# Optimization experiments

Measured on AMD Instinct MI355X. Metric: run time of the kernel, lower is better.

## Reference

```python
import jax, jax.numpy as jnp
import numpy as np

B, S, D, H = 2, 2048, 768, 12
HD = D // H


def setup_inputs() -> dict:
    key = jax.random.key(0)
    ks = jax.random.split(key, 11)
    scale = 1.0 / np.sqrt(D)
    return {
        "query": jax.random.normal(ks[0], (B, S, D), jnp.float32),
        "key_": jax.random.normal(ks[1], (B, S, D), jnp.float32),
        "value": jax.random.normal(ks[2], (B, S, D), jnp.float32),
        "Wq": jax.random.normal(ks[3], (D, D), jnp.float32) * scale,
        "bq": jnp.zeros((D,), jnp.float32),
        "Wk": jax.random.normal(ks[4], (D, D), jnp.float32) * scale,
        "bk": jnp.zeros((D,), jnp.float32),
        "Wv": jax.random.normal(ks[5], (D, D), jnp.float32) * scale,
        "bv": jnp.zeros((D,), jnp.float32),
        "Wo": jax.random.normal(ks[6], (D, D), jnp.float32) * scale,
        "bo": jnp.zeros((D,), jnp.float32),
    }


def reference(query, key_, value, Wq, bq, Wk, bk, Wv, bv, Wo, bo):
    # Linear projections (W stored as [in, out]); dropout = identity (eval)
    def split_heads(x):
        # [B, S, D] -> [B, H, S, HD]
        return x.reshape(B, S, H, HD).transpose(0, 2, 1, 3)

    Q = split_heads(query @ Wq + bq)
    K = split_heads(key_ @ Wk + bk)
    V = split_heads(value @ Wv + bv)

    inv_sqrt_dk = 1.0 / jnp.sqrt(jnp.asarray(HD, Q.dtype))
    score = jnp.einsum("bhqd,bhkd->bhqk", Q, K) * inv_sqrt_dk  # [B,H,S,S]
    prob = jax.nn.softmax(score, axis=-1)  # source bug: mask is never applied
    out = jnp.einsum("bhqk,bhkd->bhqd", prob, V)  # [B,H,S,HD]
    out = out.transpose(0, 2, 1, 3).reshape(B, S, D)
    return out @ Wo + bo
```

## Files before the change

### kernel.cpp

```cpp
#include <hip/hip_runtime.h>
#include <hip/hip_bf16.h>

#define BB 2
#define SS 2048
#define DDIM 768
#define NH 12
#define HD 64
#define MTOT (BB*SS)

constexpr float QSCALE = 0.125f * 1.44269504088896340736f;

typedef __bf16 bf16_t;
typedef __bf16 bf16x8 __attribute__((ext_vector_type(8)));
typedef __bf16 bf16x4 __attribute__((ext_vector_type(4)));
typedef float  f32x4  __attribute__((ext_vector_type(4)));

static __device__ __forceinline__ f32x4 mfma16(bf16x8 a, bf16x8 b, f32x4 c) {
    return __builtin_amdgcn_mfma_f32_16x16x32_bf16(a, b, c, 0, 0, 0);
}

typedef __attribute__((address_space(3))) unsigned int lds_u32;
typedef __attribute__((address_space(1))) const unsigned int glob_u32;
static __device__ __forceinline__ void gload16(const bf16_t* g, bf16_t* l) {
    __builtin_amdgcn_global_load_lds((glob_u32*)g, (lds_u32*)l, 16, 0, 0);
}

__global__ __launch_bounds__(256) void prep_all(
    const float* __restrict__ Wq, const float* __restrict__ Wk,
    const float* __restrict__ Wv, const float* __restrict__ Wo,
    const float* __restrict__ q, const float* __restrict__ k_,
    bf16_t* __restrict__ Wt, bf16_t* __restrict__ Xb)
{
    const int z = blockIdx.z, tid = threadIdx.x;
    if (z < 4) {
        if (blockIdx.x >= 24 || blockIdx.y >= 24) return;
        __shared__ float tile[32][33];
        const float* W = (z == 0) ? Wq : (z == 1) ? Wk : (z == 2) ? Wv : Wo;
        int n0 = blockIdx.x * 32, k0 = blockIdx.y * 32;
        int tx = tid & 31, ty = tid >> 5;
#pragma unroll
        for (int i = 0; i < 4; i++) {
            int k = ty + i * 8;
            tile[k][tx] = W[(size_t)(k0 + k) * DDIM + n0 + tx];
        }
        __syncthreads();
        bf16_t* out = Wt + (size_t)z * DDIM * DDIM;
#pragma unroll
        for (int i = 0; i < 4; i++) {
            int n = ty + i * 8;
            out[(size_t)(n0 + n) * DDIM + k0 + tx] = (bf16_t)tile[tx][n];
        }
    } else {
        const float* src = (z == 4) ? q : k_;
        size_t base = ((size_t)(blockIdx.y * 48 + blockIdx.x)) * 2048 + (size_t)tid * 8;
        f32x4 v0 = *(const f32x4*)&src[base];
        f32x4 v1 = *(const f32x4*)&src[base + 4];
        bf16x8 o;
#pragma unroll
        for (int i = 0; i < 4; i++) { o[i] = (bf16_t)v0[i]; o[i + 4] = (bf16_t)v1[i]; }
        *(bf16x8*)&Xb[(size_t)(z - 4) * MTOT * DDIM + base] = o;
    }
}

__global__ __launch_bounds__(256) void gemm_qkv(
    const bf16_t* __restrict__ Xb, const float* __restrict__ vf,
    const float* __restrict__ bq, const float* __restrict__ bk, const float* __restrict__ bv,
    const bf16_t* __restrict__ Wt,
    bf16_t* __restrict__ Q, bf16_t* __restrict__ K, bf16_t* __restrict__ Vtg)
{
    __shared__ alignas(16) bf16_t As[128 * 32];
    __shared__ alignas(16) bf16_t Bs[128 * 32];
    const int z = blockIdx.z;
    const int m0 = blockIdx.y * 128, n0 = blockIdx.x * 128;
    const int tid = threadIdx.x, lane = tid & 63, w = tid >> 6;
    const int wm = (w >> 1) * 64, wn = (w & 1) * 64;
    const int quad = lane >> 4, l15 = lane & 15;

    const bf16_t* A  = Xb + (size_t)z * (MTOT * DDIM);
    const bf16_t* Bt = Wt + (size_t)z * (DDIM * DDIM);
    const int srow = w * 32 + (lane >> 2);
    const int sg   = ((lane & 3) ^ ((lane >> 3) & 3)) * 8;
    bf16_t* AsW = &As[w * 1024];
    bf16_t* BsW = &Bs[w * 1024];
    const int frow = tid >> 1, fhalf = tid & 1;

    f32x4 acc[4][4];
#pragma unroll
    for (int mt = 0; mt < 4; mt++)
#pragma unroll
        for (int nt = 0; nt < 4; nt++) { f32x4 zz = {0.f,0.f,0.f,0.f}; acc[mt][nt] = zz; }

    const int aslot = (quad ^ ((l15 >> 1) & 3)) * 8;

    for (int k0 = 0; k0 < DDIM; k0 += 32) {
        __syncthreads();
        if (z < 2) {
            const bf16_t* Ag = A + (size_t)(m0 + srow) * DDIM + k0 + sg;
            gload16(Ag, AsW);
            gload16(Ag + (size_t)16 * DDIM, AsW + 512);
        } else {
            const float* src = vf + (size_t)(m0 + frow) * DDIM + k0 + fhalf * 16;
            f32x4 v0 = *(const f32x4*)(src);
            f32x4 v1 = *(const f32x4*)(src + 4);
            f32x4 v2 = *(const f32x4*)(src + 8);
            f32x4 v3 = *(const f32x4*)(src + 12);
            bf16x8 o0, o1;
#pragma unroll
            for (int i = 0; i < 4; i++) {
                o0[i] = (bf16_t)v0[i]; o0[i + 4] = (bf16_t)v1[i];
                o1[i] = (bf16_t)v2[i]; o1[i + 4] = (bf16_t)v3[i];
            }
            int sw = (frow >> 1) & 3;
            *(bf16x8*)&As[frow * 32 + ((2 * fhalf)     ^ sw) * 8] = o0;
            *(bf16x8*)&As[frow * 32 + ((2 * fhalf + 1) ^ sw) * 8] = o1;
        }
        {
            const bf16_t* Bg = Bt + (size_t)(n0 + srow) * DDIM + k0 + sg;
            gload16(Bg, BsW);
            gload16(Bg + (size_t)16 * DDIM, BsW + 512);
        }
        __syncthreads();

        bf16x8 a[4], b[4];
#pragma unroll
        for (int mt = 0; mt < 4; mt++)
            a[mt] = *(const bf16x8*)&As[(wm + mt * 16 + l15) * 32 + aslot];
#pragma unroll
        for (int nt = 0; nt < 4; nt++)
            b[nt] = *(const bf16x8*)&Bs[(wn + nt * 16 + l15) * 32 + aslot];
#pragma unroll
        for (int mt = 0; mt < 4; mt++)
#pragma unroll
            for (int nt = 0; nt < 4; nt++)
                acc[mt][nt] = mfma16(a[mt], b[nt], acc[mt][nt]);
    }

    const float* bias = (z == 0) ? bq : (z == 1) ? bk : bv;
    float bvals[4];
#pragma unroll
    for (int nt = 0; nt < 4; nt++)
        bvals[nt] = bias[n0 + wn + nt * 16 + l15];

    if (z == 2) {
#pragma unroll
        for (int mt = 0; mt < 4; mt++) {
            int row0 = m0 + wm + mt * 16 + quad * 4;
#pragma unroll
            for (int nt = 0; nt < 4; nt++) {
                int col = n0 + wn + nt * 16 + l15;
                bf16x4 pk;
#pragma unroll
                for (int r = 0; r < 4; r++) pk[r] = (bf16_t)(acc[mt][nt][r] + bvals[nt]);
                *(bf16x4*)&Vtg[(size_t)col * MTOT + row0] = pk;
            }
        }
    } else {
        bf16_t* C = (z == 0) ? Q : K;
        float scale = (z == 0) ? QSCALE : 1.0f;
#pragma unroll
        for (int mt = 0; mt < 4; mt++) {
            int row0 = m0 + wm + mt * 16 + quad * 4;
#pragma unroll
            for (int nt = 0; nt < 4; nt++) {
                int col = n0 + wn + nt * 16 + l15;
#pragma unroll
                for (int r = 0; r < 4; r++)
                    C[(size_t)(row0 + r) * DDIM + col] = (bf16_t)((acc[mt][nt][r] + bvals[nt]) * scale);
            }
        }
    }
}

__global__ __launch_bounds__(256) void gemm_out(
    const bf16_t* __restrict__ Ab, const bf16_t* __restrict__ Bt,
    const float* __restrict__ bo, float* __restrict__ out)
{
    __shared__ alignas(16) bf16_t As[128 * 32];
    __shared__ alignas(16) bf16_t Bs[128 * 32];
    const int m0 = blockIdx.y * 128, n0 = blockIdx.x * 128;
    const int tid = threadIdx.x, lane = tid & 63, w = tid >> 6;
    const int wm = (w >> 1) * 64, wn = (w & 1) * 64;
    const int quad = lane >> 4, l15 = lane & 15;
    const int srow = w * 32 + (lane >> 2);
    const int sg   = ((lane & 3) ^ ((lane >> 3) & 3)) * 8;
    bf16_t* AsW = &As[w * 1024];
    bf16_t* BsW = &Bs[w * 1024];

    f32x4 acc[4][4];
#pragma unroll
    for (int mt = 0; mt < 4; mt++)
#pragma unroll
        for (int nt = 0; nt < 4; nt++) { f32x4 zz = {0.f,0.f,0.f,0.f}; acc[mt][nt] = zz; }

    const int aslot = (quad ^ ((l15 >> 1) & 3)) * 8;

    for (int k0 = 0; k0 < DDIM; k0 += 32) {
        __syncthreads();
        const bf16_t* Ag = Ab + (size_t)(m0 + srow) * DDIM + k0 + sg;
        gload16(Ag, AsW);
        gload16(Ag + (size_t)16 * DDIM, AsW + 512);
        const bf16_t* Bg = Bt + (size_t)(n0 + srow) * DDIM + k0 + sg;
        gload16(Bg, BsW);
        gload16(Bg + (size_t)16 * DDIM, BsW + 512);
        __syncthreads();

        bf16x8 a[4], b[4];
#pragma unroll
        for (int mt = 0; mt < 4; mt++)
            a[mt] = *(const bf16x8*)&As[(wm + mt * 16 + l15) * 32 + aslot];
#pragma unroll
        for (int nt = 0; nt < 4; nt++)
            b[nt] = *(const bf16x8*)&Bs[(wn + nt * 16 + l15) * 32 + aslot];
#pragma unroll
        for (int mt = 0; mt < 4; mt++)
#pragma unroll
            for (int nt = 0; nt < 4; nt++)
                acc[mt][nt] = mfma16(a[mt], b[nt], acc[mt][nt]);
    }

    float bvals[4];
#pragma unroll
    for (int nt = 0; nt < 4; nt++)
        bvals[nt] = bo[n0 + wn + nt * 16 + l15];
#pragma unroll
    for (int mt = 0; mt < 4; mt++) {
        int row0 = m0 + wm + mt * 16 + quad * 4;
#pragma unroll
        for (int nt = 0; nt < 4; nt++) {
            int col = n0 + wn + nt * 16 + l15;
#pragma unroll
            for (int r = 0; r < 4; r++)
                out[(size_t)(row0 + r) * DDIM + col] = acc[mt][nt][r] + bvals[nt];
        }
    }
}

__global__ __launch_bounds__(256) void attn_kernel(
    const bf16_t* __restrict__ Qb, const bf16_t* __restrict__ Kb,
    const bf16_t* __restrict__ Vtg, bf16_t* __restrict__ Ab)
{
    const int id = blockIdx.x;
    const int hb = id % 24, qi = id / 24;
    const int h = hb % NH, b = hb / NH;
    const int q0 = qi * 64;
    const int tid = threadIdx.x, lane = tid & 63, w = tid >> 6;
    const int quad = lane >> 4, l15 = lane & 15;

    __shared__ union {
        struct {
            alignas(16) bf16_t Ps[64][144];
        } a;
        struct {
            alignas(16) float Obuf[2][64][68];
            float Lb[4][64];
        } m;
    } u;

    bf16x8 qf[4][2];
#pragma unroll
    for (int qt = 0; qt < 4; qt++) {
        const bf16_t* src = Qb + (size_t)(b * SS + q0 + qt * 16 + l15) * DDIM + h * HD;
#pragma unroll
        for (int kh = 0; kh < 2; kh++)
            qf[qt][kh] = *(const bf16x8*)(src + kh * 32 + quad * 8);
    }

    f32x4 o[4][4];
#pragma unroll
    for (int dt = 0; dt < 4; dt++)
#pragma unroll
        for (int qt = 0; qt < 4; qt++) { f32x4 z = {0.f,0.f,0.f,0.f}; o[dt][qt] = z; }
    float l_s[4];
#pragma unroll
    for (int qt = 0; qt < 4; qt++) l_s[qt] = 0.f;

    const bf16_t* kfrag = Kb + (size_t)(b * SS + w * 32 + l15) * DDIM + h * HD + quad * 8;
    const bf16_t* vfrag = Vtg + (size_t)(h * HD + l15) * MTOT + b * SS + w * 32 + quad * 8;

    for (int kt0 = 0; kt0 < SS; kt0 += 128) {
        f32x4 s_[2][4];
#pragma unroll
        for (int kt = 0; kt < 2; kt++) {
            const bf16_t* kr = kfrag + (size_t)(kt0 + kt * 16) * DDIM;
            bf16x8 ak0 = *(const bf16x8*)(kr);
            bf16x8 ak1 = *(const bf16x8*)(kr + 32);
#pragma unroll
            for (int qt = 0; qt < 4; qt++) {
                f32x4 z = {0.f,0.f,0.f,0.f};
                z = mfma16(ak0, qf[qt][0], z);
                z = mfma16(ak1, qf[qt][1], z);
                s_[kt][qt] = z;
            }
        }

#pragma unroll
        for (int qt = 0; qt < 4; qt++) {
            float rs = l_s[qt];
#pragma unroll
            for (int kt = 0; kt < 2; kt++) {
                bf16x4 pk;
#pragma unroll
                for (int r = 0; r < 4; r++) {
                    float p = __builtin_amdgcn_exp2f(s_[kt][qt][r]);
                    rs += p;
                    pk[r] = (bf16_t)p;
                }
                *(bf16x4*)&u.a.Ps[qt * 16 + l15][w * 32 + kt * 16 + quad * 4] = pk;
            }
            l_s[qt] = rs;
        }

        bf16x8 av8[4], bp[4];
#pragma unroll
        for (int dt = 0; dt < 4; dt++)
            av8[dt] = *(const bf16x8*)(vfrag + (size_t)(dt * 16) * MTOT + kt0);
#pragma unroll
        for (int qt = 0; qt < 4; qt++)
            bp[qt] = *(const bf16x8*)&u.a.Ps[qt * 16 + l15][w * 32 + quad * 8];
#pragma unroll
        for (int dt = 0; dt < 4; dt++)
#pragma unroll
            for (int qt = 0; qt < 4; qt++)
                o[dt][qt] = mfma16(av8[dt], bp[qt], o[dt][qt]);
    }

#pragma unroll
    for (int qt = 0; qt < 4; qt++) {
        float rs = l_s[qt];
        rs += __shfl_xor(rs, 16, 64);
        rs += __shfl_xor(rs, 32, 64);
        l_s[qt] = rs;
    }
    __syncthreads();
    if (quad == 0) {
#pragma unroll
        for (int qt = 0; qt < 4; qt++)
            u.m.Lb[w][qt * 16 + l15] = l_s[qt];
    }
    __syncthreads();
    float lstar[4];
#pragma unroll
    for (int qt = 0; qt < 4; qt++) {
        int q = qt * 16 + l15;
        lstar[qt] = u.m.Lb[0][q] + u.m.Lb[1][q] + u.m.Lb[2][q] + u.m.Lb[3][q];
    }
    if (w >= 2) {
        float* dst = &u.m.Obuf[w - 2][lane][0];
#pragma unroll
        for (int dt = 0; dt < 4; dt++)
#pragma unroll
            for (int qt = 0; qt < 4; qt++)
                *(f32x4*)(dst + (dt * 4 + qt) * 4) = o[dt][qt];
    }
    __syncthreads();
    if (w < 2) {
        const float* src = &u.m.Obuf[w][lane][0];
#pragma unroll
        for (int dt = 0; dt < 4; dt++)
#pragma unroll
            for (int qt = 0; qt < 4; qt++)
                o[dt][qt] += *(const f32x4*)(src + (dt * 4 + qt) * 4);
    }
    __syncthreads();
    if (w == 1) {
        float* dst = &u.m.Obuf[0][lane][0];
#pragma unroll
        for (int dt = 0; dt < 4; dt++)
#pragma unroll
            for (int qt = 0; qt < 4; qt++)
                *(f32x4*)(dst + (dt * 4 + qt) * 4) = o[dt][qt];
    }
    __syncthreads();
    if (w == 0) {
        const float* src = &u.m.Obuf[0][lane][0];
#pragma unroll
        for (int dt = 0; dt < 4; dt++)
#pragma unroll
            for (int qt = 0; qt < 4; qt++)
                o[dt][qt] += *(const f32x4*)(src + (dt * 4 + qt) * 4);
#pragma unroll
        for (int qt = 0; qt < 4; qt++) {
            float inv = 1.f / lstar[qt];
            size_t rbase = (size_t)(b * SS + q0 + qt * 16 + l15) * DDIM + h * HD;
#pragma unroll
            for (int dt = 0; dt < 4; dt++) {
                bf16x4 pk;
#pragma unroll
                for (int r = 0; r < 4; r++) pk[r] = (bf16_t)(o[dt][qt][r] * inv);
                *(bf16x4*)&Ab[rbase + dt * 16 + quad * 4] = pk;
            }
        }
    }
}

extern "C" void kernel_launch(void* const* d_in, const int* in_sizes, int n_in,
                              void* d_out, int out_size, void* d_ws, size_t ws_size,
                              hipStream_t stream)
{
    const float* q  = (const float*)d_in[0];
    const float* k  = (const float*)d_in[1];
    const float* v  = (const float*)d_in[2];
    const float* Wq = (const float*)d_in[3];
    const float* bq = (const float*)d_in[4];
    const float* Wk = (const float*)d_in[5];
    const float* bk = (const float*)d_in[6];
    const float* Wv = (const float*)d_in[7];
    const float* bv = (const float*)d_in[8];
    const float* Wo = (const float*)d_in[9];
    const float* bo = (const float*)d_in[10];
    float* out = (float*)d_out;

    bf16_t* Wt  = (bf16_t*)d_ws;
    bf16_t* Xb  = Wt + (size_t)4 * DDIM * DDIM;
    bf16_t* Qs  = Xb + (size_t)2 * MTOT * DDIM;
    bf16_t* Ks  = Qs + (size_t)MTOT * DDIM;
    bf16_t* Vtg = Ks + (size_t)MTOT * DDIM;
    bf16_t* Ab  = Xb;

    prep_all<<<dim3(48, 32, 6), 256, 0, stream>>>(Wq, Wk, Wv, Wo, q, k, Wt, Xb);
    gemm_qkv<<<dim3(6, 32, 3), 256, 0, stream>>>(Xb, v, bq, bk, bv, Wt, Qs, Ks, Vtg);
    attn_kernel<<<dim3((SS / 64) * NH * BB), 256, 0, stream>>>(Qs, Ks, Vtg, Ab);
    gemm_out<<<dim3(6, 32), 256, 0, stream>>>(Ab, Wt + (size_t)3 * DDIM * DDIM, bo, out);
}
```

Before: 213.6 us.

## Fuse fp32→bf16 input conversion into QKV GEMM and software-pipeline attention loop

The separate pass that converted query and key activations to bf16 is dropped. The QKV GEMM now reads fp32 for all three projections and converts them in registers, as it already did for value. The attention loop is also software-pipelined: the P·V product for the previous key tile is issued alongside the QK^T for the current tile, with V fragments prefetched one iteration ahead. The fused conversion removes a full write-then-read round trip of the activations but drops the async global_load_lds path for Q/K, and the pipelining raises register pressure.

```diff
diff --git a/kernel.cpp b/kernel.cpp
--- a/kernel.cpp
+++ b/kernel.cpp
@@ -25,45 +25,32 @@
     __builtin_amdgcn_global_load_lds((glob_u32*)g, (lds_u32*)l, 16, 0, 0);
 }
 
-__global__ __launch_bounds__(256) void prep_all(
+__global__ __launch_bounds__(256) void prep_w(
     const float* __restrict__ Wq, const float* __restrict__ Wk,
     const float* __restrict__ Wv, const float* __restrict__ Wo,
-    const float* __restrict__ q, const float* __restrict__ k_,
-    bf16_t* __restrict__ Wt, bf16_t* __restrict__ Xb)
+    bf16_t* __restrict__ Wt)
 {
     const int z = blockIdx.z, tid = threadIdx.x;
-    if (z < 4) {
-        if (blockIdx.x >= 24 || blockIdx.y >= 24) return;
-        __shared__ float tile[32][33];
-        const float* W = (z == 0) ? Wq : (z == 1) ? Wk : (z == 2) ? Wv : Wo;
-        int n0 = blockIdx.x * 32, k0 = blockIdx.y * 32;
-        int tx = tid & 31, ty = tid >> 5;
-#pragma unroll
-        for (int i = 0; i < 4; i++) {
-            int k = ty + i * 8;
-            tile[k][tx] = W[(size_t)(k0 + k) * DDIM + n0 + tx];
-        }
-        __syncthreads();
-        bf16_t* out = Wt + (size_t)z * DDIM * DDIM;
-#pragma unroll
-        for (int i = 0; i < 4; i++) {
-            int n = ty + i * 8;
-            out[(size_t)(n0 + n) * DDIM + k0 + tx] = (bf16_t)tile[tx][n];
-        }
-    } else {
-        const float* src = (z == 4) ? q : k_;
-        size_t base = ((size_t)(blockIdx.y * 48 + blockIdx.x)) * 2048 + (size_t)tid * 8;
-        f32x4 v0 = *(const f32x4*)&src[base];
-        f32x4 v1 = *(const f32x4*)&src[base + 4];
-        bf16x8 o;
-#pragma unroll
-        for (int i = 0; i < 4; i++) { o[i] = (bf16_t)v0[i]; o[i + 4] = (bf16_t)v1[i]; }
-        *(bf16x8*)&Xb[(size_t)(z - 4) * MTOT * DDIM + base] = o;
+    __shared__ float tile[32][33];
+    const float* W = (z == 0) ? Wq : (z == 1) ? Wk : (z == 2) ? Wv : Wo;
+    int n0 = blockIdx.x * 32, k0 = blockIdx.y * 32;
+    int tx = tid & 31, ty = tid >> 5;
+#pragma unroll
+    for (int i = 0; i < 4; i++) {
+        int k = ty + i * 8;
+        tile[k][tx] = W[(size_t)(k0 + k) * DDIM + n0 + tx];
+    }
+    __syncthreads();
+    bf16_t* out = Wt + (size_t)z * DDIM * DDIM;
+#pragma unroll
+    for (int i = 0; i < 4; i++) {
+        int n = ty + i * 8;
+        out[(size_t)(n0 + n) * DDIM + k0 + tx] = (bf16_t)tile[tx][n];
     }
 }
 
 __global__ __launch_bounds__(256) void gemm_qkv(
-    const bf16_t* __restrict__ Xb, const float* __restrict__ vf,
+    const float* __restrict__ qf_, const float* __restrict__ kf_, const float* __restrict__ vf_,
     const float* __restrict__ bq, const float* __restrict__ bk, const float* __restrict__ bv,
     const bf16_t* __restrict__ Wt,
     bf16_t* __restrict__ Q, bf16_t* __restrict__ K, bf16_t* __restrict__ Vtg)
@@ -76,11 +63,10 @@
     const int wm = (w >> 1) * 64, wn = (w & 1) * 64;
     const int quad = lane >> 4, l15 = lane & 15;
 
-    const bf16_t* A  = Xb + (size_t)z * (MTOT * DDIM);
+    const float* A = (z == 0) ? qf_ : (z == 1) ? kf_ : vf_;
     const bf16_t* Bt = Wt + (size_t)z * (DDIM * DDIM);
     const int srow = w * 32 + (lane >> 2);
     const int sg   = ((lane & 3) ^ ((lane >> 3) & 3)) * 8;
-    bf16_t* AsW = &As[w * 1024];
     bf16_t* BsW = &Bs[w * 1024];
     const int frow = tid >> 1, fhalf = tid & 1;
 
@@ -94,12 +80,8 @@
 
     for (int k0 = 0; k0 < DDIM; k0 += 32) {
         __syncthreads();
-        if (z < 2) {
-            const bf16_t* Ag = A + (size_t)(m0 + srow) * DDIM + k0 + sg;
-            gload16(Ag, AsW);
-            gload16(Ag + (size_t)16 * DDIM, AsW + 512);
-        } else {
-            const float* src = vf + (size_t)(m0 + frow) * DDIM + k0 + fhalf * 16;
+        {
+            const float* src = A + (size_t)(m0 + frow) * DDIM + k0 + fhalf * 16;
             f32x4 v0 = *(const f32x4*)(src);
             f32x4 v1 = *(const f32x4*)(src + 4);
             f32x4 v2 = *(const f32x4*)(src + 8);
@@ -277,22 +259,25 @@
     const bf16_t* kfrag = Kb + (size_t)(b * SS + w * 32 + l15) * DDIM + h * HD + quad * 8;
     const bf16_t* vfrag = Vtg + (size_t)(h * HD + l15) * MTOT + b * SS + w * 32 + quad * 8;
 
-    for (int kt0 = 0; kt0 < SS; kt0 += 128) {
+    bf16x8 vp[4];
+#pragma unroll
+    for (int dt = 0; dt < 4; dt++)
+        vp[dt] = *(const bf16x8*)(vfrag + (size_t)(dt * 16) * MTOT);
+    {
         f32x4 s_[2][4];
 #pragma unroll
         for (int kt = 0; kt < 2; kt++) {
-            const bf16_t* kr = kfrag + (size_t)(kt0 + kt * 16) * DDIM;
+            const bf16_t* kr = kfrag + (size_t)(kt * 16) * DDIM;
             bf16x8 ak0 = *(const bf16x8*)(kr);
             bf16x8 ak1 = *(const bf16x8*)(kr + 32);
 #pragma unroll
             for (int qt = 0; qt < 4; qt++) {
-                f32x4 z = {0.f,0.f,0.f,0.f};
-                z = mfma16(ak0, qf[qt][0], z);
-                z = mfma16(ak1, qf[qt][1], z);
-                s_[kt][qt] = z;
-            }
-        }
-
+                f32x4 zz = {0.f,0.f,0.f,0.f};
+                zz = mfma16(ak0, qf[qt][0], zz);
+                zz = mfma16(ak1, qf[qt][1], zz);
+                s_[kt][qt] = zz;
+            }
+        }
 #pragma unroll
         for (int qt = 0; qt < 4; qt++) {
             float rs = l_s[qt];
@@ -309,19 +294,72 @@
             }
             l_s[qt] = rs;
         }
-
-        bf16x8 av8[4], bp[4];
-#pragma unroll
-        for (int dt = 0; dt < 4; dt++)
-            av8[dt] = *(const bf16x8*)(vfrag + (size_t)(dt * 16) * MTOT + kt0);
+    }
+
+    for (int kt0 = 128; kt0 < SS; kt0 += 128) {
+        bf16x8 ak[2][2];
+#pragma unroll
+        for (int kt = 0; kt < 2; kt++) {
+            const bf16_t* kr = kfrag + (size_t)(kt0 + kt * 16) * DDIM;
+            ak[kt][0] = *(const bf16x8*)(kr);
+            ak[kt][1] = *(const bf16x8*)(kr + 32);
+        }
+        bf16x8 bp[4];
 #pragma unroll
         for (int qt = 0; qt < 4; qt++)
             bp[qt] = *(const bf16x8*)&u.a.Ps[qt * 16 + l15][w * 32 + quad * 8];
-#pragma unroll
-        for (int dt = 0; dt < 4; dt++)
-#pragma unroll
-            for (int qt = 0; qt < 4; qt++)
-                o[dt][qt] = mfma16(av8[dt], bp[qt], o[dt][qt]);
+        bf16x8 vc[4];
+#pragma unroll
+        for (int dt = 0; dt < 4; dt++)
+            vc[dt] = *(const bf16x8*)(vfrag + (size_t)(dt * 16) * MTOT + kt0);
+
+#pragma unroll
+        for (int dt = 0; dt < 4; dt++)
+#pragma unroll
+            for (int qt = 0; qt < 4; qt++)
+                o[dt][qt] = mfma16(vp[dt], bp[qt], o[dt][qt]);
+
+        f32x4 s_[2][4];
+#pragma unroll
+        for (int kt = 0; kt < 2; kt++) {
+#pragma unroll
+            for (int qt = 0; qt < 4; qt++) {
+                f32x4 zz = {0.f,0.f,0.f,0.f};
+                zz = mfma16(ak[kt][0], qf[qt][0], zz);
+                zz = mfma16(ak[kt][1], qf[qt][1], zz);
+                s_[kt][qt] = zz;
+            }
+        }
+#pragma unroll
+        for (int qt = 0; qt < 4; qt++) {
+            float rs = l_s[qt];
+#pragma unroll
+            for (int kt = 0; kt < 2; kt++) {
+                bf16x4 pk;
+#pragma unroll
+                for (int r = 0; r < 4; r++) {
+                    float p = __builtin_amdgcn_exp2f(s_[kt][qt][r]);
+                    rs += p;
+                    pk[r] = (bf16_t)p;
+                }
+                *(bf16x4*)&u.a.Ps[qt * 16 + l15][w * 32 + kt * 16 + quad * 4] = pk;
+            }
+            l_s[qt] = rs;
+        }
+#pragma unroll
+        for (int dt = 0; dt < 4; dt++) vp[dt] = vc[dt];
+    }
+
+    {
+        bf16x8 bp[4];
+#pragma unroll
+        for (int qt = 0; qt < 4; qt++)
+            bp[qt] = *(const bf16x8*)&u.a.Ps[qt * 16 + l15][w * 32 + quad * 8];
+#pragma unroll
+        for (int dt = 0; dt < 4; dt++)
+#pragma unroll
+            for (int qt = 0; qt < 4; qt++)
+                o[dt][qt] = mfma16(vp[dt], bp[qt], o[dt][qt]);
     }
 
 #pragma unroll
@@ -411,14 +449,13 @@
     float* out = (float*)d_out;
 
     bf16_t* Wt  = (bf16_t*)d_ws;
-    bf16_t* Xb  = Wt + (size_t)4 * DDIM * DDIM;
-    bf16_t* Qs  = Xb + (size_t)2 * MTOT * DDIM;
+    bf16_t* Qs  = Wt + (size_t)4 * DDIM * DDIM;
     bf16_t* Ks  = Qs + (size_t)MTOT * DDIM;
     bf16_t* Vtg = Ks + (size_t)MTOT * DDIM;
-    bf16_t* Ab  = Xb;
-
-    prep_all<<<dim3(48, 32, 6), 256, 0, stream>>>(Wq, Wk, Wv, Wo, q, k, Wt, Xb);
-    gemm_qkv<<<dim3(6, 32, 3), 256, 0, stream>>>(Xb, v, bq, bk, bv, Wt, Qs, Ks, Vtg);
+    bf16_t* Ab  = Vtg + (size_t)MTOT * DDIM;
+
+    prep_w<<<dim3(24, 24, 4), 256, 0, stream>>>(Wq, Wk, Wv, Wo, Wt);
+    gemm_qkv<<<dim3(6, 32, 3), 256, 0, stream>>>(q, k, v, bq, bk, bv, Wt, Qs, Ks, Vtg);
     attn_kernel<<<dim3((SS / 64) * NH * BB), 256, 0, stream>>>(Qs, Ks, Vtg, Ab);
     gemm_out<<<dim3(6, 32), 256, 0, stream>>>(Ab, Wt + (size_t)3 * DDIM * DDIM, bo, out);
 }
```

Result: slower. 225.9 us (+5.8%).

## Double-buffer LDS tiles in the QKV and output GEMMs

Applied to the files above, without the earlier changes.

Both projection GEMMs now keep two LDS buffers for the A and B tiles. The next K-slice is prefetched into the idle buffer while MFMAs run on the current one, so each iteration needs one barrier instead of two. This is meant to hide global-to-LDS load latency behind matrix compute. It doubles LDS use per block to 32 KB, and for the fp32 V input the synchronous load-and-convert path overlaps little, since the stores into LDS must finish before the compute starts.

```diff
diff --git a/kernel.cpp b/kernel.cpp
--- a/kernel.cpp
+++ b/kernel.cpp
@@ -68,8 +68,8 @@
     const bf16_t* __restrict__ Wt,
     bf16_t* __restrict__ Q, bf16_t* __restrict__ K, bf16_t* __restrict__ Vtg)
 {
-    __shared__ alignas(16) bf16_t As[128 * 32];
-    __shared__ alignas(16) bf16_t Bs[128 * 32];
+    __shared__ alignas(16) bf16_t As[2][128 * 32];
+    __shared__ alignas(16) bf16_t Bs[2][128 * 32];
     const int z = blockIdx.z;
     const int m0 = blockIdx.y * 128, n0 = blockIdx.x * 128;
     const int tid = threadIdx.x, lane = tid & 63, w = tid >> 6;
@@ -80,9 +80,8 @@
     const bf16_t* Bt = Wt + (size_t)z * (DDIM * DDIM);
     const int srow = w * 32 + (lane >> 2);
     const int sg   = ((lane & 3) ^ ((lane >> 3) & 3)) * 8;
-    bf16_t* AsW = &As[w * 1024];
-    bf16_t* BsW = &Bs[w * 1024];
     const int frow = tid >> 1, fhalf = tid & 1;
+    const int aslot = (quad ^ ((l15 >> 1) & 3)) * 8;
 
     f32x4 acc[4][4];
 #pragma unroll
@@ -90,44 +89,69 @@
 #pragma unroll
         for (int nt = 0; nt < 4; nt++) { f32x4 zz = {0.f,0.f,0.f,0.f}; acc[mt][nt] = zz; }
 
-    const int aslot = (quad ^ ((l15 >> 1) & 3)) * 8;
-
-    for (int k0 = 0; k0 < DDIM; k0 += 32) {
+    if (z < 2) {
+        const bf16_t* Ag = A + (size_t)(m0 + srow) * DDIM + sg;
+        gload16(Ag, &As[0][w * 1024]);
+        gload16(Ag + (size_t)16 * DDIM, &As[0][w * 1024 + 512]);
+    } else {
+        const float* src = vf + (size_t)(m0 + frow) * DDIM + fhalf * 16;
+        f32x4 v0 = *(const f32x4*)(src);
+        f32x4 v1 = *(const f32x4*)(src + 4);
+        f32x4 v2 = *(const f32x4*)(src + 8);
+        f32x4 v3 = *(const f32x4*)(src + 12);
+        bf16x8 o0, o1;
+#pragma unroll
+        for (int i = 0; i < 4; i++) {
+            o0[i] = (bf16_t)v0[i]; o0[i + 4] = (bf16_t)v1[i];
+            o1[i] = (bf16_t)v2[i]; o1[i + 4] = (bf16_t)v3[i];
+        }
+        int sw = (frow >> 1) & 3;
+        *(bf16x8*)&As[0][frow * 32 + ((2 * fhalf)     ^ sw) * 8] = o0;
+        *(bf16x8*)&As[0][frow * 32 + ((2 * fhalf + 1) ^ sw) * 8] = o1;
+    }
+    {
+        const bf16_t* Bg = Bt + (size_t)(n0 + srow) * DDIM + sg;
+        gload16(Bg, &Bs[0][w * 1024]);
+        gload16(Bg + (size_t)16 * DDIM, &Bs[0][w * 1024 + 512]);
+    }
+
+    for (int j = 0; j < 24; j++) {
+        const int cur = j & 1, nxt = cur ^ 1;
         __syncthreads();
-        if (z < 2) {
-            const bf16_t* Ag = A + (size_t)(m0 + srow) * DDIM + k0 + sg;
-            gload16(Ag, AsW);
-            gload16(Ag + (size_t)16 * DDIM, AsW + 512);
-        } else {
-            const float* src = vf + (size_t)(m0 + frow) * DDIM + k0 + fhalf * 16;
-            f32x4 v0 = *(const f32x4*)(src);
-            f32x4 v1 = *(const f32x4*)(src + 4);
-            f32x4 v2 = *(const f32x4*)(src + 8);
-            f32x4 v3 = *(const f32x4*)(src + 12);
-            bf16x8 o0, o1;
-#pragma unroll
-            for (int i = 0; i < 4; i++) {
-                o0[i] = (bf16_t)v0[i]; o0[i + 4] = (bf16_t)v1[i];
-                o1[i] = (bf16_t)v2[i]; o1[i + 4] = (bf16_t)v3[i];
-            }
-            int sw = (frow >> 1) & 3;
-            *(bf16x8*)&As[frow * 32 + ((2 * fhalf)     ^ sw) * 8] = o0;
-            *(bf16x8*)&As[frow * 32 + ((2 * fhalf + 1) ^ sw) * 8] = o1;
-        }
-        {
+        if (j < 23) {
+            const int k0 = (j + 1) * 32;
+            if (z < 2) {
+                const bf16_t* Ag = A + (size_t)(m0 + srow) * DDIM + k0 + sg;
+                gload16(Ag, &As[nxt][w * 1024]);
+                gload16(Ag + (size_t)16 * DDIM, &As[nxt][w * 1024 + 512]);
+            } else {
+                const float* src = vf + (size_t)(m0 + frow) * DDIM + k0 + fhalf * 16;
+                f32x4 v0 = *(const f32x4*)(src);
+                f32x4 v1 = *(const f32x4*)(src + 4);
+                f32x4 v2 = *(const f32x4*)(src + 8);
+                f32x4 v3 = *(const f32x4*)(src + 12);
+                bf16x8 o0, o1;
+#pragma unroll
+                for (int i = 0; i < 4; i++) {
+                    o0[i] = (bf16_t)v0[i]; o0[i + 4] = (bf16_t)v1[i];
+                    o1[i] = (bf16_t)v2[i]; o1[i + 4] = (bf16_t)v3[i];
+                }
+                int sw = (frow >> 1) & 3;
+                *(bf16x8*)&As[nxt][frow * 32 + ((2 * fhalf)     ^ sw) * 8] = o0;
+                *(bf16x8*)&As[nxt][frow * 32 + ((2 * fhalf + 1) ^ sw) * 8] = o1;
+            }
             const bf16_t* Bg = Bt + (size_t)(n0 + srow) * DDIM + k0 + sg;
-            gload16(Bg, BsW);
-            gload16(Bg + (size_t)16 * DDIM, BsW + 512);
-        }
-        __syncthreads();
+            gload16(Bg, &Bs[nxt][w * 1024]);
+            gload16(Bg + (size_t)16 * DDIM, &Bs[nxt][w * 1024 + 512]);
+        }
 
         bf16x8 a[4], b[4];
 #pragma unroll
         for (int mt = 0; mt < 4; mt++)
-            a[mt] = *(const bf16x8*)&As[(wm + mt * 16 + l15) * 32 + aslot];
+            a[mt] = *(const bf16x8*)&As[cur][(wm + mt * 16 + l15) * 32 + aslot];
 #pragma unroll
         for (int nt = 0; nt < 4; nt++)
-            b[nt] = *(const bf16x8*)&Bs[(wn + nt * 16 + l15) * 32 + aslot];
+            b[nt] = *(const bf16x8*)&Bs[cur][(wn + nt * 16 + l15) * 32 + aslot];
 #pragma unroll
         for (int mt = 0; mt < 4; mt++)
 #pragma unroll
@@ -175,16 +199,15 @@
     const bf16_t* __restrict__ Ab, const bf16_t* __restrict__ Bt,
     const float* __restrict__ bo, float* __restrict__ out)
 {
-    __shared__ alignas(16) bf16_t As[128 * 32];
-    __shared__ alignas(16) bf16_t Bs[128 * 32];
+    __shared__ alignas(16) bf16_t As[2][128 * 32];
+    __shared__ alignas(16) bf16_t Bs[2][128 * 32];
     const int m0 = blockIdx.y * 128, n0 = blockIdx.x * 128;
     const int tid = threadIdx.x, lane = tid & 63, w = tid >> 6;
     const int wm = (w >> 1) * 64, wn = (w & 1) * 64;
     const int quad = lane >> 4, l15 = lane & 15;
     const int srow = w * 32 + (lane >> 2);
     const int sg   = ((lane & 3) ^ ((lane >> 3) & 3)) * 8;
-    bf16_t* AsW = &As[w * 1024];
-    bf16_t* BsW = &Bs[w * 1024];
+    const int aslot = (quad ^ ((l15 >> 1) & 3)) * 8;
 
     f32x4 acc[4][4];
 #pragma unroll
@@ -192,25 +215,35 @@
 #pragma unroll
         for (int nt = 0; nt < 4; nt++) { f32x4 zz = {0.f,0.f,0.f,0.f}; acc[mt][nt] = zz; }
 
-    const int aslot = (quad ^ ((l15 >> 1) & 3)) * 8;
-
-    for (int k0 = 0; k0 < DDIM; k0 += 32) {
+    {
+        const bf16_t* Ag = Ab + (size_t)(m0 + srow) * DDIM + sg;
+        gload16(Ag, &As[0][w * 1024]);
+        gload16(Ag + (size_t)16 * DDIM, &As[0][w * 1024 + 512]);
+        const bf16_t* Bg = Bt + (size_t)(n0 + srow) * DDIM + sg;
+        gload16(Bg, &Bs[0][w * 1024]);
+        gload16(Bg + (size_t)16 * DDIM, &Bs[0][w * 1024 + 512]);
+    }
+
+    for (int j = 0; j < 24; j++) {
+        const int cur = j & 1, nxt = cur ^ 1;
         __syncthreads();
-        const bf16_t* Ag = Ab + (size_t)(m0 + srow) * DDIM + k0 + sg;
-        gload16(Ag, AsW);
-        gload16(Ag + (size_t)16 * DDIM, AsW + 512);
-        const bf16_t* Bg = Bt + (size_t)(n0 + srow) * DDIM + k0 + sg;
-        gload16(Bg, BsW);
-        gload16(Bg + (size_t)16 * DDIM, BsW + 512);
-        __syncthreads();
+        if (j < 23) {
+            const int k0 = (j + 1) * 32;
+            const bf16_t* Ag = Ab + (size_t)(m0 + srow) * DDIM + k0 + sg;
+            gload16(Ag, &As[nxt][w * 1024]);
+            gload16(Ag + (size_t)16 * DDIM, &As[nxt][w * 1024 + 512]);
+            const bf16_t* Bg = Bt + (size_t)(n0 + srow) * DDIM + k0 + sg;
+            gload16(Bg, &Bs[nxt][w * 1024]);
+            gload16(Bg + (size_t)16 * DDIM, &Bs[nxt][w * 1024 + 512]);
+        }
 
         bf16x8 a[4], b[4];
 #pragma unroll
         for (int mt = 0; mt < 4; mt++)
-            a[mt] = *(const bf16x8*)&As[(wm + mt * 16 + l15) * 32 + aslot];
+            a[mt] = *(const bf16x8*)&As[cur][(wm + mt * 16 + l15) * 32 + aslot];
 #pragma unroll
         for (int nt = 0; nt < 4; nt++)
-            b[nt] = *(const bf16x8*)&Bs[(wn + nt * 16 + l15) * 32 + aslot];
+            b[nt] = *(const bf16x8*)&Bs[cur][(wn + nt * 16 + l15) * 32 + aslot];
 #pragma unroll
         for (int mt = 0; mt < 4; mt++)
 #pragma unroll
```

New measurement: 217.8 us. About the same (+2.0%).
